# Kernel optimization log

Measured on AMD Instinct MI355X. Metric: run time of the kernel, lower is better.

The kernel has to match this reference:

```python
import jax, jax.numpy as jnp
import numpy as np

K = 51  # separable kernel taps
PAD = (K - 1) // 2  # 25


def _lerp_axis(a, n_in, n_out, axis):
    # 1D bilinear resample with align_corners=True semantics
    pos = jnp.arange(n_out, dtype=jnp.float32) * (float(n_in - 1) / float(n_out - 1))
    lo = jnp.floor(pos).astype(jnp.int32)
    hi = jnp.minimum(lo + 1, n_in - 1)
    w = (pos - lo.astype(jnp.float32)).astype(a.dtype)
    shp = [1] * a.ndim
    shp[axis] = n_out
    w = w.reshape(shp)
    return jnp.take(a, lo, axis=axis) * (1 - w) + jnp.take(a, hi, axis=axis) * w


def upsample2x_align_corners(x):
    B, C, H, W = x.shape
    x = _lerp_axis(x, H, 2 * H, 2)
    x = _lerp_axis(x, W, 2 * W, 3)
    return x


def conv3x3(x, w, b):
    y = jax.lax.conv_general_dilated(
        x, w, window_strides=(1, 1), padding=((1, 1), (1, 1)),
        dimension_numbers=('NCHW', 'OIHW', 'NCHW'))
    return y + b[None, :, None, None]


def kernel_block(x, w1, b1, w2, b2, w3, b3):
    h = upsample2x_align_corners(x)
    h = jax.nn.relu(conv3x3(h, w1, b1))
    h = jax.nn.relu(conv3x3(h, w2, b2))
    h = jax.nn.relu(conv3x3(h, w3, b3))
    return h  # [B, 51, H, W]


def sep_conv(img, kv, kh):
    # img: [B,C,H+K-1,W+K-1]; kv, kh: [B,K,H,W]
    # out[b,c,y,x] = sum_{i,j} img[b,c,y+i,x+j] * kv[b,i,y,x] * kh[b,j,y,x]
    B, C, Hp, Wp = img.shape
    H, W = kv.shape[2], kv.shape[3]
    # vertical sliding windows: [B,C,K,H,Wp]
    vwin = jnp.stack([img[:, :, i:i + H, :] for i in range(K)], axis=2)
    out = jnp.zeros((B, C, H, W), img.dtype)
    for j in range(K):  # static loop over K taps
        t = jnp.einsum('bciyx,biyx->bcyx', vwin[:, :, :, :, j:j + W], kv)
        out = out + t * kh[:, j][:, None]
    return out


def setup_inputs() -> dict:
    key = jax.random.key(0)
    ks = jax.random.split(key, 9)
    B, Cf, Hh, Wh = 4, 64, 128, 128  # feature map (half res)
    H, W = 2 * Hh, 2 * Wh
    x = jax.random.normal(ks[0], (B, Cf, Hh, Wh), jnp.float32)
    i1 = jax.random.normal(ks[1], (B, 3, H + 2 * PAD, W + 2 * PAD), jnp.float32)
    i2 = jax.random.normal(ks[2], (B, 3, H + 2 * PAD, W + 2 * PAD), jnp.float32)
    s = 0.05
    W1 = jax.random.normal(ks[3], (4, K, Cf, 3, 3), jnp.float32) * s
    B1 = jax.random.normal(ks[4], (4, K), jnp.float32) * s
    W2 = jax.random.normal(ks[5], (4, K, K, 3, 3), jnp.float32) * s
    B2 = jax.random.normal(ks[6], (4, K), jnp.float32) * s
    W3 = jax.random.normal(ks[7], (4, K, K, 3, 3), jnp.float32) * s
    B3 = jax.random.normal(ks[8], (4, K), jnp.float32) * s
    return {'x': x, 'i1': i1, 'i2': i2,
            'W1': W1, 'B1': B1, 'W2': W2, 'B2': B2, 'W3': W3, 'B3': B3}


def reference(x, i1, i2, W1, B1, W2, B2, W3, B3):
    kernels = [kernel_block(x, W1[k], B1[k], W2[k], B2[k], W3[k], B3[k])
               for k in range(4)]
    k1v, k1h, k2v, k2h = kernels
    y = sep_conv(i1, k1v, k1h) + sep_conv(i2, k2v, k2h)
    return y
```

## Files before the change

kernel.cpp:

```cpp
#include <hip/hip_runtime.h>
#include <stdint.h>

#define HH 128
#define H 256
#define W 256
#define KK 51
#define HIMG 306
#define WIMG 306
#define CF 64
#define BB 4
#define HWN (H * W)
#define CHAIN ((size_t)HWN * 64)

typedef short bhalf8 __attribute__((ext_vector_type(8)));
typedef float f32x4 __attribute__((ext_vector_type(4)));

__device__ inline uint16_t f2bf(float f) {
    uint32_t u = __builtin_bit_cast(uint32_t, f);
    u += 0x7FFF + ((u >> 16) & 1);
    return (uint16_t)(u >> 16);
}
__device__ inline float bf2f(uint16_t h) {
    uint32_t u = ((uint32_t)h) << 16;
    return __builtin_bit_cast(float, u);
}

__global__ __launch_bounds__(256) void upsample_cvt(const float* __restrict__ xin,
                                                    uint16_t* __restrict__ upT) {
    const int z = blockIdx.z;
    xin += (size_t)z * CF * HH * HH;
    upT += (size_t)z * CHAIN;
    __shared__ float SU[2][64][19];
    const int y = blockIdx.x, x0 = blockIdx.y * 32;
    const float s = 127.f / 255.f;
    float py = y * s; int ly = (int)py; int hy = min(ly + 1, 127); float wy = py - (float)ly;
    int lx0 = (int)(x0 * s);
    for (int t = threadIdx.x; t < 2 * 64 * 18; t += 256) {
        int col = t % 18; int c = (t / 18) & 63; int row = t / (18 * 64);
        int sy = row ? hy : ly;
        int sx = min(lx0 + col, 127);
        SU[row][c][col] = xin[((size_t)c * 128 + sy) * 128 + sx];
    }
    __syncthreads();
    const int xl = threadIdx.x & 31, cg = threadIdx.x >> 5;
    const int x = x0 + xl;
    float px = x * s; int lx = (int)px; float wx = px - (float)lx;
    int lxl = lx - lx0;
    int hxl = min(lx + 1, 127) - lx0;
    uint32_t d[4];
#pragma unroll
    for (int q4 = 0; q4 < 4; ++q4) {
        uint32_t two[2];
#pragma unroll
        for (int e = 0; e < 2; ++e) {
            int c = cg * 8 + q4 * 2 + e;
            float v00 = SU[0][c][lxl], v01 = SU[0][c][hxl];
            float v10 = SU[1][c][lxl], v11 = SU[1][c][hxl];
            float a = v00 * (1.f - wy) + v10 * wy;
            float b = v01 * (1.f - wy) + v11 * wy;
            two[e] = f2bf(a * (1.f - wx) + b * wx);
        }
        d[q4] = two[0] | (two[1] << 16);
    }
    uint4 v = {d[0], d[1], d[2], d[3]};
    *(uint4*)(upT + ((size_t)y * W + x) * 64 + cg * 8) = v;
}

__global__ void wprep(const float* __restrict__ wsrc, uint16_t* __restrict__ wdst, int cin_act) {
    int g = blockIdx.x * 256 + threadIdx.x;
    if (g >= 4 * 9 * 4 * 2 * 64) return;
    int lane = g & 63;
    int q = g >> 6;
    int ch = q & 1; q >>= 1;
    int m = q & 3; q >>= 2;
    int tap = q % 9;
    int k = q / 9;
    int co = m * 16 + (lane & 15);
    int ci0 = ch * 32 + (lane >> 4) * 8;
    uint32_t d[4];
#pragma unroll
    for (int p = 0; p < 4; ++p) {
        uint32_t w2[2];
#pragma unroll
        for (int e = 0; e < 2; ++e) {
            int ci = ci0 + p * 2 + e;
            float v = 0.f;
            if (co < KK && ci < cin_act)
                v = wsrc[((size_t)(k * KK + co) * cin_act + ci) * 9 + tap];
            w2[e] = f2bf(v);
        }
        d[p] = w2[0] | (w2[1] << 16);
    }
    uint4 v = {d[0], d[1], d[2], d[3]};
    *(uint4*)(wdst + (size_t)g * 8) = v;
}

__global__ __launch_bounds__(256, 2)
void conv_mfma(const uint16_t* __restrict__ in, const uint16_t* __restrict__ wp,
               const float* __restrict__ bias, uint16_t* __restrict__ out,
               size_t in_cstride, size_t in_bstride, int kbase) {
    const int z = blockIdx.z;
    const int k = kbase + (z & 3);
    in  += (size_t)(z & 3) * in_cstride + (size_t)(z >> 2) * in_bstride;
    out += (size_t)z * CHAIN;
    const int y0 = blockIdx.x * 4;
    const int x0 = blockIdx.y * 64;
    const int tid = threadIdx.x;
    const int lane = tid & 63;
    const int wv = tid >> 6;
    const int y = y0 + wv;

    __shared__ uint4 lds[6 * 66 * 8];

    uint4 stg[13];
    int   dsti[13];
#pragma unroll
    for (int it = 0; it < 13; ++it) {
        int t = tid + it * 256;
        bool ok = t < 6 * 66 * 8;
        int c = t & 7;
        int q = t >> 3;
        int xl = q % 66;
        int r = q / 66;
        int yg = y0 - 1 + r;
        int xg = x0 + xl - 1;
        uint4 v = {0u, 0u, 0u, 0u};
        if (ok && (unsigned)yg < H && (unsigned)xg < W)
            v = *(const uint4*)(in + (((size_t)yg * W + xg) * 64 + c * 8));
        stg[it] = v;
        dsti[it] = ok ? (q * 8 + (c ^ (xl & 7))) : -1;
    }
#pragma unroll
    for (int it = 0; it < 13; ++it)
        if (dsti[it] >= 0) lds[dsti[it]] = stg[it];
    __syncthreads();

    f32x4 acc[4][4];
#pragma unroll
    for (int m = 0; m < 4; ++m)
#pragma unroll
        for (int n = 0; n < 4; ++n)
            acc[m][n] = (f32x4){0.f, 0.f, 0.f, 0.f};

    const int l4 = lane & 15, g = lane >> 4;
    __builtin_amdgcn_s_setprio(1);
#pragma unroll
    for (int chf = 0; chf < 2; ++chf) {
#pragma unroll
        for (int tap = 0; tap < 9; ++tap) {
            const int ky = tap / 3, kx = tap % 3;
            bhalf8 afr[4];
#pragma unroll
            for (int m = 0; m < 4; ++m)
                afr[m] = *(const bhalf8*)(wp + ((((size_t)(k * 9 + tap) * 4 + m) * 2 + chf) * 64 + lane) * 8);
            const int rrow = wv + ky;
#pragma unroll
            for (int n = 0; n < 4; ++n) {
                int xl = n * 16 + l4 + kx;
                int slot = (chf * 4 + g) ^ (xl & 7);
                bhalf8 bfr = *(const bhalf8*)&lds[((size_t)rrow * 66 + xl) * 8 + slot];
#pragma unroll
                for (int m = 0; m < 4; ++m)
                    acc[m][n] = __builtin_amdgcn_mfma_f32_16x16x32_bf16(afr[m], bfr, acc[m][n], 0, 0, 0);
            }
        }
    }
    __builtin_amdgcn_s_setprio(0);

    __syncthreads();
    ushort* ST = (ushort*)lds + wv * 4096;
    float bv[4][4];
#pragma unroll
    for (int m = 0; m < 4; ++m)
#pragma unroll
        for (int r = 0; r < 4; ++r) {
            int co = m * 16 + g * 4 + r;
            bv[m][r] = (co < KK) ? bias[k * KK + co] : 0.f;
        }

#pragma unroll
    for (int m = 0; m < 4; ++m) {
#pragma unroll
        for (int nn = 0; nn < 4; ++nn) {
            int xl = nn * 16 + l4;
            uint32_t pk[2];
#pragma unroll
            for (int hh = 0; hh < 2; ++hh) {
                uint32_t lo = f2bf(fmaxf(acc[m][nn][hh * 2]     + bv[m][hh * 2],     0.f));
                uint32_t hi = f2bf(fmaxf(acc[m][nn][hh * 2 + 1] + bv[m][hh * 2 + 1], 0.f));
                pk[hh] = lo | (hi << 16);
            }
            int idx = xl * 64 + ((m * 16 + g * 4) ^ ((xl & 7) << 3));
            *(uint2*)(ST + idx) = (uint2){pk[0], pk[1]};
        }
    }
    const int p8 = lane >> 3;
    const int ch = lane & 7;
#pragma unroll
    for (int it = 0; it < 8; ++it) {
        int px = it * 8 + p8;
        uint4 v = *(const uint4*)(ST + px * 64 + ((ch ^ (px & 7)) << 3));
        *(uint4*)(out + (((size_t)y * W + x0 + px) * 64 + ch * 8)) = v;
    }
}

__global__ __launch_bounds__(256, 2)
void sepconv3(const float* __restrict__ img,
              const uint16_t* __restrict__ kvT, const uint16_t* __restrict__ khT,
              float* __restrict__ out, int accum) {
    __shared__ uint4 SB[320 * 8];
    __shared__ float SC[4][16 * 83];
    const int y = blockIdx.x, c = blockIdx.y, z = blockIdx.z;
    const int tid = threadIdx.x, lane = tid & 63, wv = tid >> 6;
    const float* ip = img + (size_t)(z * 3 + c) * HIMG * WIMG;
    kvT += (size_t)z * 4 * CHAIN;
    khT += (size_t)z * 4 * CHAIN;

    for (int task = tid; task < 40 * 64; task += 256) {
        int i = task & 63;
        int u0 = (task >> 6) * 8;
        float f[8];
        bool rowok = (i <= 50);
        const float* rp = ip + (size_t)(y + i) * WIMG;
#pragma unroll
        for (int e2 = 0; e2 < 4; ++e2) {
            int u = u0 + e2 * 2;
            float2 v2 = (rowok && u < WIMG) ? *(const float2*)(rp + u) : float2{0.f, 0.f};
            f[e2 * 2] = v2.x; f[e2 * 2 + 1] = v2.y;
        }
#pragma unroll
        for (int e = 0; e < 8; ++e) {
            int u = u0 + e;
            *((ushort*)SB + u * 64 + (((i >> 3) ^ (u & 7)) << 3) + (i & 7)) = f2bf(f[e]);
        }
    }
    __syncthreads();

    const int l4 = lane & 15, g = lane >> 4;
    for (int xt = 0; xt < 4; ++xt) {
        const int x0 = (wv * 4 + xt) * 16;
        const int xpix = x0 + l4;
        bhalf8 a0 = *(const bhalf8*)(kvT + ((size_t)y * W + xpix) * 64 + g * 8);
        bhalf8 a1 = *(const bhalf8*)(kvT + ((size_t)y * W + xpix) * 64 + 32 + g * 8);
        f32x4 acc[5];
#pragma unroll
        for (int nt = 0; nt < 5; ++nt) acc[nt] = (f32x4){0.f, 0.f, 0.f, 0.f};
#pragma unroll
        for (int nt = 0; nt < 5; ++nt) {
            int u = x0 + nt * 16 + l4;
            bhalf8 b0 = *(const bhalf8*)((ushort*)SB + u * 64 + ((g ^ (u & 7)) << 3));
            acc[nt] = __builtin_amdgcn_mfma_f32_16x16x32_bf16(a0, b0, acc[nt], 0, 0, 0);
            bhalf8 b1 = *(const bhalf8*)((ushort*)SB + u * 64 + (((4 + g) ^ (u & 7)) << 3));
            acc[nt] = __builtin_amdgcn_mfma_f32_16x16x32_bf16(a1, b1, acc[nt], 0, 0, 0);
        }
#pragma unroll
        for (int nt = 0; nt < 5; ++nt)
#pragma unroll
            for (int r = 0; r < 4; ++r)
                SC[wv][(g * 4 + r) * 83 + nt * 16 + l4] = acc[nt][r];

        const uint16_t* khp = khT + ((size_t)y * W + xpix) * 64;
        float partial = 0.f;
#pragma unroll
        for (int jj = 0; jj < 13; ++jj) {
            int j = g * 13 + jj;
            if (j < KK)
                partial = fmaf(SC[wv][l4 * 83 + l4 + j], bf2f(khp[j]), partial);
        }
        partial += __shfl_xor(partial, 16);
        partial += __shfl_xor(partial, 32);
        if (g == 0) {
            size_t oi = ((size_t)(z * 3 + c) * H + y) * W + xpix;
            if (accum) out[oi] += partial;
            else       out[oi] = partial;
        }
    }
}

extern "C" void kernel_launch(void* const* d_in, const int* in_sizes, int n_in,
                              void* d_out, int out_size, void* d_ws, size_t ws_size,
                              hipStream_t stream) {
    const float* x  = (const float*)d_in[0];
    const float* i1 = (const float*)d_in[1];
    const float* i2 = (const float*)d_in[2];
    const float* W1 = (const float*)d_in[3];
    const float* B1 = (const float*)d_in[4];
    const float* W2 = (const float*)d_in[5];
    const float* B2 = (const float*)d_in[6];
    const float* W3 = (const float*)d_in[7];
    const float* B3 = (const float*)d_in[8];
    float* out = (float*)d_out;

    char* wsb = (char*)d_ws;
    const size_t IMGB = CHAIN * 2;
    const size_t WPN  = 4 * 9 * 4 * 2 * 64 * 8;

    uint16_t* wp1 = (uint16_t*)d_out;
    uint16_t* wp2 = wp1 + WPN;
    uint16_t* wp3 = wp2 + WPN;
    wprep<<<72, 256, 0, stream>>>(W1, wp1, CF);
    wprep<<<72, 256, 0, stream>>>(W2, wp2, KK);
    wprep<<<72, 256, 0, stream>>>(W3, wp3, KK);

    if (ws_size >= 32 * IMGB) {
        uint16_t* A = (uint16_t*)wsb;
        uint16_t* Bp = (uint16_t*)(wsb + 16 * IMGB);
        uint16_t* upT = Bp + 12 * CHAIN;

        upsample_cvt<<<dim3(H, 8, BB), 256, 0, stream>>>(x, upT);
        conv_mfma<<<dim3(64, 4, 16), 256, 0, stream>>>(upT, wp1, B1, A, 0, CHAIN, 0);
        conv_mfma<<<dim3(64, 4, 16), 256, 0, stream>>>(A,  wp2, B2, Bp, CHAIN, 4 * CHAIN, 0);
        conv_mfma<<<dim3(64, 4, 16), 256, 0, stream>>>(Bp, wp3, B3, A,  CHAIN, 4 * CHAIN, 0);
        sepconv3<<<dim3(H, 3, BB), 256, 0, stream>>>(i1, A,             A + CHAIN,     out, 0);
        sepconv3<<<dim3(H, 3, BB), 256, 0, stream>>>(i2, A + 2 * CHAIN, A + 3 * CHAIN, out, 1);
    } else if (ws_size >= 13 * IMGB) {
        uint16_t* r1  = (uint16_t*)wsb;
        uint16_t* r2  = (uint16_t*)(wsb + 4 * IMGB);
        uint16_t* r3  = (uint16_t*)(wsb + 8 * IMGB);
        uint16_t* upT = (uint16_t*)(wsb + 12 * IMGB);
        for (int b = 0; b < BB; ++b) {
            upsample_cvt<<<dim3(H, 8, 1), 256, 0, stream>>>(x + (size_t)b * CF * HH * HH, upT);
            conv_mfma<<<dim3(64, 4, 4), 256, 0, stream>>>(upT, wp1, B1, r1, 0, 0, 0);
            conv_mfma<<<dim3(64, 4, 4), 256, 0, stream>>>(r1, wp2, B2, r2, CHAIN, 0, 0);
            conv_mfma<<<dim3(64, 4, 4), 256, 0, stream>>>(r2, wp3, B3, r3, CHAIN, 0, 0);
            for (int p = 0; p < 2; ++p) {
                const float* img = (p ? i2 : i1) + (size_t)b * 3 * HIMG * WIMG;
                sepconv3<<<dim3(H, 3, 1), 256, 0, stream>>>(img,
                        r3 + (size_t)(2 * p) * CHAIN, r3 + (size_t)(2 * p + 1) * CHAIN,
                        out + (size_t)b * 3 * HWN, p);
            }
        }
    } else {
        uint16_t* upT = (uint16_t*)wsb;
        uint16_t* t1  = (uint16_t*)(wsb + 1 * IMGB);
        uint16_t* t2  = (uint16_t*)(wsb + 3 * IMGB);
        uint16_t* t3  = (uint16_t*)(wsb + 5 * IMGB);
        for (int b = 0; b < BB; ++b) {
            upsample_cvt<<<dim3(H, 8, 1), 256, 0, stream>>>(x + (size_t)b * CF * HH * HH, upT);
            for (int p = 0; p < 2; ++p) {
                conv_mfma<<<dim3(64, 4, 2), 256, 0, stream>>>(upT, wp1, B1, t1, 0, 0, 2 * p);
                conv_mfma<<<dim3(64, 4, 2), 256, 0, stream>>>(t1, wp2, B2, t2, CHAIN, 0, 2 * p);
                conv_mfma<<<dim3(64, 4, 2), 256, 0, stream>>>(t2, wp3, B3, t3, CHAIN, 0, 2 * p);
                const float* img = (p ? i2 : i1) + (size_t)b * 3 * HIMG * WIMG;
                sepconv3<<<dim3(H, 3, 1), 256, 0, stream>>>(img, t3, t3 + CHAIN,
                        out + (size_t)b * 3 * HWN, p);
            }
        }
    }
}
```

Before: 542.4 us.

## Fuse conv2 and conv3 with halo recompute; share input tile across kernels in conv1

Adds conv1_mfma, which loads the upsampled input tile into LDS once and loops over all four kernel-block weight sets, so the input is not re-read for each one. Adds conv23_mfma, which computes conv2 over a one-pixel-larger halo tile into LDS and then runs conv3 straight from LDS. This removes the global write and read of the intermediate conv2 activation and one launch. The cost is halo recompute (30 16-pixel tiles where 24 are needed), larger LDS use and 512-thread blocks, which may lower occupancy.

```diff
diff --git a/kernel.cpp b/kernel.cpp
--- a/kernel.cpp
+++ b/kernel.cpp
@@ -23,6 +23,9 @@
 __device__ inline float bf2f(uint16_t h) {
     uint32_t u = ((uint32_t)h) << 16;
     return __builtin_bit_cast(float, u);
+}
+__device__ inline bhalf8 aload(const uint16_t* wp, int k, int tap, int m, int chf, int lane) {
+    return *(const bhalf8*)(wp + ((((size_t)(k * 9 + tap) * 4 + m) * 2 + chf) * 64 + lane) * 8);
 }
 
 __global__ __launch_bounds__(256) void upsample_cvt(const float* __restrict__ xin,
@@ -95,6 +98,286 @@
     *(uint4*)(wdst + (size_t)g * 8) = v;
 }
 
+__global__ __launch_bounds__(512)
+void conv1_mfma(const uint16_t* __restrict__ in, const uint16_t* __restrict__ wp,
+                const float* __restrict__ bias, uint16_t* __restrict__ out) {
+    const int b = blockIdx.z;
+    in  += (size_t)b * CHAIN;
+    out += (size_t)b * 4 * CHAIN;
+    const int y0 = blockIdx.x * 4;
+    const int x0 = blockIdx.y * 64;
+    const int tid = threadIdx.x;
+    const int lane = tid & 63;
+    const int wv = tid >> 6;
+    const int l4 = lane & 15, g = lane >> 4;
+
+    __shared__ uint4 lds[6 * 66 * 8 + 2048];
+
+    uint4 stg[7]; int dsti[7];
+#pragma unroll
+    for (int it = 0; it < 7; ++it) {
+        int t = tid + it * 512;
+        bool ok = t < 6 * 66 * 8;
+        int c = t & 7;
+        int q = t >> 3;
+        int xl = q % 66;
+        int r = q / 66;
+        int yg = y0 - 1 + r;
+        int xg = x0 + xl - 1;
+        uint4 v = {0u, 0u, 0u, 0u};
+        if (ok && (unsigned)yg < H && (unsigned)xg < W)
+            v = *(const uint4*)(in + (((size_t)yg * W + xg) * 64 + c * 8));
+        stg[it] = v;
+        dsti[it] = ok ? (q * 8 + (c ^ (xl & 7))) : -1;
+    }
+#pragma unroll
+    for (int it = 0; it < 7; ++it)
+        if (dsti[it] >= 0) lds[dsti[it]] = stg[it];
+    __syncthreads();
+
+    const int row = wv & 3;
+    const int nh = (wv >> 2) * 2;
+    const int y = y0 + row;
+    ushort* ST = (ushort*)(lds + 6 * 66 * 8) + wv * 2048;
+
+    for (int k = 0; k < 4; ++k) {
+        f32x4 acc[4][2];
+#pragma unroll
+        for (int m = 0; m < 4; ++m)
+#pragma unroll
+            for (int nn = 0; nn < 2; ++nn) acc[m][nn] = (f32x4){0.f, 0.f, 0.f, 0.f};
+
+        __builtin_amdgcn_s_setprio(1);
+#pragma unroll
+        for (int chf = 0; chf < 2; ++chf)
+#pragma unroll
+            for (int tap = 0; tap < 9; ++tap) {
+                bhalf8 afr[4];
+#pragma unroll
+                for (int m = 0; m < 4; ++m) afr[m] = aload(wp, k, tap, m, chf, lane);
+                const int ky = tap / 3, kx = tap % 3;
+                const int rrow = row + ky;
+#pragma unroll
+                for (int nn = 0; nn < 2; ++nn) {
+                    int xl = (nh + nn) * 16 + l4 + kx;
+                    int slot = (chf * 4 + g) ^ (xl & 7);
+                    bhalf8 bfr = *(const bhalf8*)&lds[((size_t)rrow * 66 + xl) * 8 + slot];
+#pragma unroll
+                    for (int m = 0; m < 4; ++m)
+                        acc[m][nn] = __builtin_amdgcn_mfma_f32_16x16x32_bf16(afr[m], bfr, acc[m][nn], 0, 0, 0);
+                }
+            }
+        __builtin_amdgcn_s_setprio(0);
+
+#pragma unroll
+        for (int m = 0; m < 4; ++m) {
+            int co0 = m * 16 + g * 4;
+            float bvr[4];
+#pragma unroll
+            for (int r = 0; r < 4; ++r)
+                bvr[r] = (co0 + r < KK) ? bias[k * KK + co0 + r] : 0.f;
+#pragma unroll
+            for (int nn = 0; nn < 2; ++nn) {
+                int pxl = nn * 16 + l4;
+                uint32_t pk[2];
+#pragma unroll
+                for (int hh = 0; hh < 2; ++hh) {
+                    uint32_t lo = f2bf(fmaxf(acc[m][nn][hh * 2]     + bvr[hh * 2],     0.f));
+                    uint32_t hi = f2bf(fmaxf(acc[m][nn][hh * 2 + 1] + bvr[hh * 2 + 1], 0.f));
+                    pk[hh] = lo | (hi << 16);
+                }
+                int idx = pxl * 64 + (co0 ^ ((pxl & 7) << 3));
+                *(uint2*)(ST + idx) = (uint2){pk[0], pk[1]};
+            }
+        }
+        const int p8 = lane >> 3;
+        const int ch = lane & 7;
+#pragma unroll
+        for (int it = 0; it < 4; ++it) {
+            int px = it * 8 + p8;
+            uint4 v = *(const uint4*)(ST + px * 64 + ((ch ^ (px & 7)) << 3));
+            *(uint4*)(out + (size_t)k * CHAIN +
+                      (((size_t)y * W + x0 + nh * 16 + px) * 64 + ch * 8)) = v;
+        }
+    }
+}
+
+__global__ __launch_bounds__(512)
+void conv23_mfma(const uint16_t* __restrict__ in, const uint16_t* __restrict__ wpa,
+                 const uint16_t* __restrict__ wpb, const float* __restrict__ bias2,
+                 const float* __restrict__ bias3, uint16_t* __restrict__ out) {
+    const int z = blockIdx.z;
+    const int k = z & 3;
+    in  += (size_t)z * CHAIN;
+    out += (size_t)z * CHAIN;
+    const int y0 = blockIdx.x * 4;
+    const int x0 = blockIdx.y * 64;
+    const int tid = threadIdx.x;
+    const int lane = tid & 63;
+    const int wv = tid >> 6;
+    const int l4 = lane & 15, g = lane >> 4;
+
+    __shared__ uint4 SA[8 * 68 * 8];
+    __shared__ uint4 SBB[6 * 66 * 8];
+
+    uint4 stg[9]; int dsti[9];
+#pragma unroll
+    for (int it = 0; it < 9; ++it) {
+        int t = tid + it * 512;
+        bool ok = t < 8 * 68 * 8;
+        int c = t & 7;
+        int q = t >> 3;
+        int xi = q % 68;
+        int r = q / 68;
+        int yg = y0 - 2 + r;
+        int xg = x0 - 2 + xi;
+        uint4 v = {0u, 0u, 0u, 0u};
+        if (ok && (unsigned)yg < H && (unsigned)xg < W)
+            v = *(const uint4*)(in + (((size_t)yg * W + xg) * 64 + c * 8));
+        stg[it] = v;
+        dsti[it] = ok ? (q * 8 + (c ^ (xi & 7))) : -1;
+    }
+#pragma unroll
+    for (int it = 0; it < 9; ++it)
+        if (dsti[it] >= 0) SA[dsti[it]] = stg[it];
+    __syncthreads();
+
+    int rowA[4], ntA[4]; bool vA[4];
+#pragma unroll
+    for (int i = 0; i < 4; ++i) {
+        int t = wv * 4 + i;
+        vA[i] = t < 30;
+        int tt = vA[i] ? t : 0;
+        rowA[i] = tt / 5;
+        ntA[i] = tt % 5;
+    }
+    f32x4 p1[4][4];
+#pragma unroll
+    for (int i = 0; i < 4; ++i)
+#pragma unroll
+        for (int m = 0; m < 4; ++m) p1[i][m] = (f32x4){0.f, 0.f, 0.f, 0.f};
+
+    __builtin_amdgcn_s_setprio(1);
+#pragma unroll
+    for (int chf = 0; chf < 2; ++chf)
+#pragma unroll
+        for (int tap = 0; tap < 9; ++tap) {
+            bhalf8 a2[4];
+#pragma unroll
+            for (int m = 0; m < 4; ++m) a2[m] = aload(wpa, k, tap, m, chf, lane);
+            const int ky = tap / 3, kx = tap % 3;
+#pragma unroll
+            for (int i = 0; i < 4; ++i) {
+                int xi = ntA[i] * 16 + l4 + kx;
+                xi = min(xi, 67);
+                int rr = rowA[i] + ky;
+                int slot = (chf * 4 + g) ^ (xi & 7);
+                bhalf8 bfr = *(const bhalf8*)&SA[((size_t)rr * 68 + xi) * 8 + slot];
+#pragma unroll
+                for (int m = 0; m < 4; ++m)
+                    p1[i][m] = __builtin_amdgcn_mfma_f32_16x16x32_bf16(a2[m], bfr, p1[i][m], 0, 0, 0);
+            }
+        }
+    __builtin_amdgcn_s_setprio(0);
+
+    {
+        float bv2[4][4];
+#pragma unroll
+        for (int m = 0; m < 4; ++m)
+#pragma unroll
+            for (int r = 0; r < 4; ++r) {
+                int co = m * 16 + g * 4 + r;
+                bv2[m][r] = (co < KK) ? bias2[k * KK + co] : 0.f;
+            }
+        ushort* SBp = (ushort*)SBB;
+#pragma unroll
+        for (int i = 0; i < 4; ++i) {
+            int xl = ntA[i] * 16 + l4;
+            if (vA[i] && xl < 66) {
+                bool inim = ((unsigned)(y0 - 1 + rowA[i]) < H) &&
+                            ((unsigned)(x0 - 1 + xl) < W);
+#pragma unroll
+                for (int m = 0; m < 4; ++m) {
+                    int co0 = m * 16 + g * 4;
+                    uint32_t pk[2];
+#pragma unroll
+                    for (int hh = 0; hh < 2; ++hh) {
+                        uint32_t lo = f2bf(fmaxf(p1[i][m][hh * 2]     + bv2[m][hh * 2],     0.f));
+                        uint32_t hi = f2bf(fmaxf(p1[i][m][hh * 2 + 1] + bv2[m][hh * 2 + 1], 0.f));
+                        pk[hh] = lo | (hi << 16);
+                    }
+                    if (!inim) { pk[0] = 0u; pk[1] = 0u; }
+                    int idx = (rowA[i] * 66 + xl) * 64 + (co0 ^ ((xl & 7) << 3));
+                    *(uint2*)(SBp + idx) = (uint2){pk[0], pk[1]};
+                }
+            }
+        }
+    }
+    __syncthreads();
+
+    const int row2 = wv & 3;
+    const int nh = (wv >> 2) * 2;
+    const int y = y0 + row2;
+    f32x4 p2[4][2];
+#pragma unroll
+    for (int m = 0; m < 4; ++m)
+#pragma unroll
+        for (int nn = 0; nn < 2; ++nn) p2[m][nn] = (f32x4){0.f, 0.f, 0.f, 0.f};
+
+    __builtin_amdgcn_s_setprio(1);
+#pragma unroll
+    for (int chf = 0; chf < 2; ++chf)
+#pragma unroll
+        for (int tap = 0; tap < 9; ++tap) {
+            bhalf8 a3[4];
+#pragma unroll
+            for (int m = 0; m < 4; ++m) a3[m] = aload(wpb, k, tap, m, chf, lane);
+            const int ky = tap / 3, kx = tap % 3;
+            const int rrow = row2 + ky;
+#pragma unroll
+            for (int nn = 0; nn < 2; ++nn) {
+                int xl = (nh + nn) * 16 + l4 + kx;
+                int slot = (chf * 4 + g) ^ (xl & 7);
+                bhalf8 bfr = *(const bhalf8*)&SBB[((size_t)rrow * 66 + xl) * 8 + slot];
+#pragma unroll
+                for (int m = 0; m < 4; ++m)
+                    p2[m][nn] = __builtin_amdgcn_mfma_f32_16x16x32_bf16(a3[m], bfr, p2[m][nn], 0, 0, 0);
+            }
+        }
+    __builtin_amdgcn_s_setprio(0);
+
+    ushort* ST = (ushort*)SA + wv * 2048;
+#pragma unroll
+    for (int m = 0; m < 4; ++m) {
+        int co0 = m * 16 + g * 4;
+        float bvr[4];
+#pragma unroll
+        for (int r = 0; r < 4; ++r)
+            bvr[r] = (co0 + r < KK) ? bias3[k * KK + co0 + r] : 0.f;
+#pragma unroll
+        for (int nn = 0; nn < 2; ++nn) {
+            int pxl = nn * 16 + l4;
+            uint32_t pk[2];
+#pragma unroll
+            for (int hh = 0; hh < 2; ++hh) {
+                uint32_t lo = f2bf(fmaxf(p2[m][nn][hh * 2]     + bvr[hh * 2],     0.f));
+                uint32_t hi = f2bf(fmaxf(p2[m][nn][hh * 2 + 1] + bvr[hh * 2 + 1], 0.f));
+                pk[hh] = lo | (hi << 16);
+            }
+            int idx = pxl * 64 + (co0 ^ ((pxl & 7) << 3));
+            *(uint2*)(ST + idx) = (uint2){pk[0], pk[1]};
+        }
+    }
+    const int p8 = lane >> 3;
+    const int ch = lane & 7;
+#pragma unroll
+    for (int it = 0; it < 4; ++it) {
+        int px = it * 8 + p8;
+        uint4 v = *(const uint4*)(ST + px * 64 + ((ch ^ (px & 7)) << 3));
+        *(uint4*)(out + (((size_t)y * W + x0 + nh * 16 + px) * 64 + ch * 8)) = v;
+    }
+}
+
 __global__ __launch_bounds__(256, 2)
 void conv_mfma(const uint16_t* __restrict__ in, const uint16_t* __restrict__ wp,
                const float* __restrict__ bias, uint16_t* __restrict__ out,
@@ -151,8 +434,7 @@
             const int ky = tap / 3, kx = tap % 3;
             bhalf8 afr[4];
 #pragma unroll
-            for (int m = 0; m < 4; ++m)
-                afr[m] = *(const bhalf8*)(wp + ((((size_t)(k * 9 + tap) * 4 + m) * 2 + chf) * 64 + lane) * 8);
+            for (int m = 0; m < 4; ++m) afr[m] = aload(wp, k, tap, m, chf, lane);
             const int rrow = wv + ky;
 #pragma unroll
             for (int n = 0; n < 4; ++n) {
@@ -303,16 +585,15 @@
     wprep<<<72, 256, 0, stream>>>(W3, wp3, KK);
 
     if (ws_size >= 32 * IMGB) {
-        uint16_t* A = (uint16_t*)wsb;
-        uint16_t* Bp = (uint16_t*)(wsb + 16 * IMGB);
-        uint16_t* upT = Bp + 12 * CHAIN;
+        uint16_t* A   = (uint16_t*)wsb;
+        uint16_t* Bb  = (uint16_t*)(wsb + 16 * IMGB);
+        uint16_t* upT = Bb + 12 * CHAIN;
 
         upsample_cvt<<<dim3(H, 8, BB), 256, 0, stream>>>(x, upT);
-        conv_mfma<<<dim3(64, 4, 16), 256, 0, stream>>>(upT, wp1, B1, A, 0, CHAIN, 0);
-        conv_mfma<<<dim3(64, 4, 16), 256, 0, stream>>>(A,  wp2, B2, Bp, CHAIN, 4 * CHAIN, 0);
-        conv_mfma<<<dim3(64, 4, 16), 256, 0, stream>>>(Bp, wp3, B3, A,  CHAIN, 4 * CHAIN, 0);
-        sepconv3<<<dim3(H, 3, BB), 256, 0, stream>>>(i1, A,             A + CHAIN,     out, 0);
-        sepconv3<<<dim3(H, 3, BB), 256, 0, stream>>>(i2, A + 2 * CHAIN, A + 3 * CHAIN, out, 1);
+        conv1_mfma<<<dim3(64, 4, BB), 512, 0, stream>>>(upT, wp1, B1, A);
+        conv23_mfma<<<dim3(64, 4, 16), 512, 0, stream>>>(A, wp2, wp3, B2, B3, Bb);
+        sepconv3<<<dim3(H, 3, BB), 256, 0, stream>>>(i1, Bb,             Bb + CHAIN,     out, 0);
+        sepconv3<<<dim3(H, 3, BB), 256, 0, stream>>>(i2, Bb + 2 * CHAIN, Bb + 3 * CHAIN, out, 1);
     } else if (ws_size >= 13 * IMGB) {
         uint16_t* r1  = (uint16_t*)wsb;
         uint16_t* r2  = (uint16_t*)(wsb + 4 * IMGB);
```

After: 639.7 us. 1.18x slower.

## Load conv halo tiles directly into LDS and remap blocks for XCD locality

Applied to the files above, without the earlier changes.

The conv_mfma halo tile is now staged with global_load_lds, which writes each 16-byte chunk straight into LDS instead of passing through registers. The XOR swizzle moves to the global source address. Out-of-bounds entries are clamped on load and then zeroed in LDS after a waitcnt. The grid is flattened to 1D and block ids are remapped so neighbouring tiles land on the same XCD (8-way interleave), which should improve L2 reuse of shared halos and weights. This frees the staging registers at the cost of a second LDS write for border tiles.

```diff
diff --git a/kernel.cpp b/kernel.cpp
--- a/kernel.cpp
+++ b/kernel.cpp
@@ -23,6 +23,14 @@
 __device__ inline float bf2f(uint16_t h) {
     uint32_t u = ((uint32_t)h) << 16;
     return __builtin_bit_cast(float, u);
+}
+__device__ inline bhalf8 aload(const uint16_t* wp, int k, int tap, int m, int chf, int lane) {
+    return *(const bhalf8*)(wp + ((((size_t)(k * 9 + tap) * 4 + m) * 2 + chf) * 64 + lane) * 8);
+}
+__device__ inline void gload_lds16(const void* g, void* l) {
+    __builtin_amdgcn_global_load_lds(
+        (const __attribute__((address_space(1))) unsigned int*)g,
+        (__attribute__((address_space(3))) unsigned int*)l, 16, 0, 0);
 }
 
 __global__ __launch_bounds__(256) void upsample_cvt(const float* __restrict__ xin,
@@ -99,12 +107,16 @@
 void conv_mfma(const uint16_t* __restrict__ in, const uint16_t* __restrict__ wp,
                const float* __restrict__ bias, uint16_t* __restrict__ out,
                size_t in_cstride, size_t in_bstride, int kbase) {
-    const int z = blockIdx.z;
+    const int wg = blockIdx.x;
+    const int id = (wg & 7) * ((int)gridDim.x >> 3) + (wg >> 3);
+    const int z = id >> 8;
+    const int rem = id & 255;
+    const int y0 = (rem & 63) * 4;
+    const int x0 = (rem >> 6) * 64;
+
     const int k = kbase + (z & 3);
     in  += (size_t)(z & 3) * in_cstride + (size_t)(z >> 2) * in_bstride;
     out += (size_t)z * CHAIN;
-    const int y0 = blockIdx.x * 4;
-    const int x0 = blockIdx.y * 64;
     const int tid = threadIdx.x;
     const int lane = tid & 63;
     const int wv = tid >> 6;
@@ -112,27 +124,31 @@
 
     __shared__ uint4 lds[6 * 66 * 8];
 
-    uint4 stg[13];
-    int   dsti[13];
+    unsigned oobmask = 0;
 #pragma unroll
     for (int it = 0; it < 13; ++it) {
         int t = tid + it * 256;
-        bool ok = t < 6 * 66 * 8;
-        int c = t & 7;
-        int q = t >> 3;
-        int xl = q % 66;
-        int r = q / 66;
-        int yg = y0 - 1 + r;
-        int xg = x0 + xl - 1;
-        uint4 v = {0u, 0u, 0u, 0u};
-        if (ok && (unsigned)yg < H && (unsigned)xg < W)
-            v = *(const uint4*)(in + (((size_t)yg * W + xg) * 64 + c * 8));
-        stg[it] = v;
-        dsti[it] = ok ? (q * 8 + (c ^ (xl & 7))) : -1;
-    }
+        if (t < 6 * 66 * 8) {
+            int c = t & 7;
+            int q = t >> 3;
+            int xl = q % 66;
+            int r = q / 66;
+            int yg = y0 - 1 + r;
+            int xg = x0 + xl - 1;
+            if ((unsigned)yg >= H || (unsigned)xg >= W) {
+                oobmask |= 1u << it;
+                yg = min(max(yg, 0), H - 1);
+                xg = min(max(xg, 0), W - 1);
+            }
+            int cs = c ^ (xl & 7);
+            gload_lds16(in + (((size_t)yg * W + xg) * 64 + cs * 8),
+                        (char*)lds + ((size_t)it * 256 + wv * 64) * 16);
+        }
+    }
+    asm volatile("s_waitcnt vmcnt(0)" ::: "memory");
 #pragma unroll
     for (int it = 0; it < 13; ++it)
-        if (dsti[it] >= 0) lds[dsti[it]] = stg[it];
+        if (oobmask & (1u << it)) lds[tid + it * 256] = (uint4){0u, 0u, 0u, 0u};
     __syncthreads();
 
     f32x4 acc[4][4];
@@ -151,8 +167,7 @@
             const int ky = tap / 3, kx = tap % 3;
             bhalf8 afr[4];
 #pragma unroll
-            for (int m = 0; m < 4; ++m)
-                afr[m] = *(const bhalf8*)(wp + ((((size_t)(k * 9 + tap) * 4 + m) * 2 + chf) * 64 + lane) * 8);
+            for (int m = 0; m < 4; ++m) afr[m] = aload(wp, k, tap, m, chf, lane);
             const int rrow = wv + ky;
 #pragma unroll
             for (int n = 0; n < 4; ++n) {
@@ -303,14 +318,14 @@
     wprep<<<72, 256, 0, stream>>>(W3, wp3, KK);
 
     if (ws_size >= 32 * IMGB) {
-        uint16_t* A = (uint16_t*)wsb;
-        uint16_t* Bp = (uint16_t*)(wsb + 16 * IMGB);
-        uint16_t* upT = Bp + 12 * CHAIN;
+        uint16_t* A   = (uint16_t*)wsb;
+        uint16_t* Bb  = (uint16_t*)(wsb + 16 * IMGB);
+        uint16_t* upT = Bb + 12 * CHAIN;
 
         upsample_cvt<<<dim3(H, 8, BB), 256, 0, stream>>>(x, upT);
-        conv_mfma<<<dim3(64, 4, 16), 256, 0, stream>>>(upT, wp1, B1, A, 0, CHAIN, 0);
-        conv_mfma<<<dim3(64, 4, 16), 256, 0, stream>>>(A,  wp2, B2, Bp, CHAIN, 4 * CHAIN, 0);
-        conv_mfma<<<dim3(64, 4, 16), 256, 0, stream>>>(Bp, wp3, B3, A,  CHAIN, 4 * CHAIN, 0);
+        conv_mfma<<<dim3(64 * 4 * 16), 256, 0, stream>>>(upT, wp1, B1, A, 0, CHAIN, 0);
+        conv_mfma<<<dim3(64 * 4 * 16), 256, 0, stream>>>(A,  wp2, B2, Bb, CHAIN, 4 * CHAIN, 0);
+        conv_mfma<<<dim3(64 * 4 * 16), 256, 0, stream>>>(Bb, wp3, B3, A,  CHAIN, 4 * CHAIN, 0);
         sepconv3<<<dim3(H, 3, BB), 256, 0, stream>>>(i1, A,             A + CHAIN,     out, 0);
         sepconv3<<<dim3(H, 3, BB), 256, 0, stream>>>(i2, A + 2 * CHAIN, A + 3 * CHAIN, out, 1);
     } else if (ws_size >= 13 * IMGB) {
@@ -320,9 +335,9 @@
         uint16_t* upT = (uint16_t*)(wsb + 12 * IMGB);
         for (int b = 0; b < BB; ++b) {
             upsample_cvt<<<dim3(H, 8, 1), 256, 0, stream>>>(x + (size_t)b * CF * HH * HH, upT);
-            conv_mfma<<<dim3(64, 4, 4), 256, 0, stream>>>(upT, wp1, B1, r1, 0, 0, 0);
-            conv_mfma<<<dim3(64, 4, 4), 256, 0, stream>>>(r1, wp2, B2, r2, CHAIN, 0, 0);
-            conv_mfma<<<dim3(64, 4, 4), 256, 0, stream>>>(r2, wp3, B3, r3, CHAIN, 0, 0);
+            conv_mfma<<<dim3(64 * 4 * 4), 256, 0, stream>>>(upT, wp1, B1, r1, 0, 0, 0);
+            conv_mfma<<<dim3(64 * 4 * 4), 256, 0, stream>>>(r1, wp2, B2, r2, CHAIN, 0, 0);
+            conv_mfma<<<dim3(64 * 4 * 4), 256, 0, stream>>>(r2, wp3, B3, r3, CHAIN, 0, 0);
             for (int p = 0; p < 2; ++p) {
                 const float* img = (p ? i2 : i1) + (size_t)b * 3 * HIMG * WIMG;
                 sepconv3<<<dim3(H, 3, 1), 256, 0, stream>>>(img,
@@ -338,9 +353,9 @@
         for (int b = 0; b < BB; ++b) {
             upsample_cvt<<<dim3(H, 8, 1), 256, 0, stream>>>(x + (size_t)b * CF * HH * HH, upT);
             for (int p = 0; p < 2; ++p) {
-                conv_mfma<<<dim3(64, 4, 2), 256, 0, stream>>>(upT, wp1, B1, t1, 0, 0, 2 * p);
-                conv_mfma<<<dim3(64, 4, 2), 256, 0, stream>>>(t1, wp2, B2, t2, CHAIN, 0, 2 * p);
-                conv_mfma<<<dim3(64, 4, 2), 256, 0, stream>>>(t2, wp3, B3, t3, CHAIN, 0, 2 * p);
+                conv_mfma<<<dim3(64 * 4 * 2), 256, 0, stream>>>(upT, wp1, B1, t1, 0, 0, 2 * p);
+                conv_mfma<<<dim3(64 * 4 * 2), 256, 0, stream>>>(t1, wp2, B2, t2, CHAIN, 0, 2 * p);
+                conv_mfma<<<dim3(64 * 4 * 2), 256, 0, stream>>>(t2, wp3, B3, t3, CHAIN, 0, 2 * p);
                 const float* img = (p ? i2 : i1) + (size_t)b * 3 * HIMG * WIMG;
                 sepconv3<<<dim3(H, 3, 1), 256, 0, stream>>>(img, t3, t3 + CHAIN,
                         out + (size_t)b * 3 * HWN, p);
```

After: 542.7 us. No clear change (+0.0%).
